# Optimization experiments

Measured on AMD Instinct MI355X. Metric: run time of the kernel, lower is better.

## Reference

```python
import jax, jax.numpy as jnp
import numpy as np

L = 4096          # total packed length
HID = 2560        # hidden_size
H = 8             # num_attention_heads
KV = 4            # num_key_value_heads
HD = 256          # head_dim
SW = 1024         # sliding_window
SCALING = 256.0 ** -0.5  # query_pre_attn_scalar ** -0.5
EPS = 1e-6
ROPE_BASE = 10000.0


def setup_inputs() -> dict:
    key = jax.random.key(0)
    ks = jax.random.split(key, 9)
    hidden_states = jax.random.normal(ks[0], (L, HID), jnp.float32)
    Wq = jax.random.normal(ks[1], (HID, H * HD), jnp.float32) * 0.02
    Wk = jax.random.normal(ks[2], (HID, KV * HD), jnp.float32) * 0.02
    Wv = jax.random.normal(ks[3], (HID, KV * HD), jnp.float32) * 0.02
    Wo = jax.random.normal(ks[4], (H * HD, HID), jnp.float32) * 0.02
    q_norm_w = jax.random.normal(ks[5], (HD,), jnp.float32) * 0.1
    k_norm_w = jax.random.normal(ks[6], (HD,), jnp.float32) * 0.1
    # 4 packed sequences of length 1024 each; positions restart per sequence
    cu_seqlens = jnp.array([0, 1024, 2048, 3072, 4096], jnp.int32)
    pos = jnp.tile(jnp.arange(1024, dtype=jnp.float32), 4)  # [L]
    inv_freq = 1.0 / (ROPE_BASE ** (jnp.arange(0, HD, 2, dtype=jnp.float32) / HD))
    freqs = pos[:, None] * inv_freq[None, :]                # [L, HD/2]
    emb = jnp.concatenate([freqs, freqs], axis=-1)          # [L, HD]
    cos, sin = jnp.cos(emb), jnp.sin(emb)
    return {"hidden_states": hidden_states, "cos": cos, "sin": sin,
            "Wq": Wq, "Wk": Wk, "Wv": Wv, "Wo": Wo,
            "q_norm_w": q_norm_w, "k_norm_w": k_norm_w,
            "cu_seqlens": cu_seqlens}


def _rotate_half(x):
    x1, x2 = x[..., : HD // 2], x[..., HD // 2:]
    return jnp.concatenate([-x2, x1], axis=-1)


def _rms_norm(x, w):
    # Gemma3RMSNorm: x * rsqrt(mean(x^2) + eps) * (1 + w)
    x32 = x.astype(jnp.float32)
    out = x32 * jax.lax.rsqrt(jnp.mean(x32 * x32, axis=-1, keepdims=True) + EPS)
    return (out * (1.0 + w.astype(jnp.float32))).astype(x.dtype)


def _packed_sliding_causal_mask(cu_seqlens, total_len):
    pos = jnp.arange(total_len)
    seq_ids = jnp.searchsorted(cu_seqlens[1:], pos, side='right')
    seq_mask = seq_ids[:, None] == seq_ids[None, :]
    dist = pos[None, :] - pos[:, None]                      # pos[j] - pos[i]
    causal = dist <= 0
    window = dist >= -(SW - 1)                              # left_window = SW - 1
    keep = seq_mask & causal & window
    return jnp.where(keep, 0.0, -jnp.inf).astype(jnp.float32)  # [L, L]


def reference(hidden_states, cos, sin, Wq, Wk, Wv, Wo, q_norm_w, k_norm_w, cu_seqlens):
    total_len = hidden_states.shape[0]
    # projections -> [n_heads, L, head_dim]
    q = (hidden_states @ Wq).reshape(total_len, H, HD).transpose(1, 0, 2)
    k = (hidden_states @ Wk).reshape(total_len, KV, HD).transpose(1, 0, 2)
    v = (hidden_states @ Wv).reshape(total_len, KV, HD).transpose(1, 0, 2)
    q = _rms_norm(q, q_norm_w)
    k = _rms_norm(k, k_norm_w)
    # RoPE (cos/sin broadcast over heads)
    q = q * cos + _rotate_half(q) * sin
    k = k * cos + _rotate_half(k) * sin
    # GQA repeat_kv: [KV, L, HD] -> [H, L, HD]
    n_rep = H // KV
    k = jnp.repeat(k, n_rep, axis=0)
    v = jnp.repeat(v, n_rep, axis=0)
    mask = _packed_sliding_causal_mask(cu_seqlens, total_len)
    scores = jnp.einsum('hqd,hkd->hqk', q, k) * SCALING + mask[None]
    attn = jax.nn.softmax(scores.astype(jnp.float32), axis=-1).astype(q.dtype)
    out = jnp.einsum('hqk,hkd->qhd', attn, v).reshape(total_len, H * HD)
    return out @ Wo  # [L, hidden]
```

## Files before the change

kernel.cpp:

```cpp
#include <hip/hip_runtime.h>
#include <hip/hip_bf16.h>

typedef unsigned short u16;
typedef float f32x4 __attribute__((ext_vector_type(4)));
typedef short bf16x8 __attribute__((ext_vector_type(8)));

__device__ __forceinline__ float bf2f(u16 u) {
    union { float f; unsigned int i; } c; c.i = ((unsigned int)u) << 16; return c.f;
}
__device__ __forceinline__ u16 f2bf(float f) {
    union { float f; unsigned int i; } c; c.f = f;
    unsigned int r = c.i + 0x7fffu + ((c.i >> 16) & 1u);
    return (u16)(r >> 16);
}
__device__ __forceinline__ void gload16(const void* g, void* l) {
    __builtin_amdgcn_global_load_lds(
        (const __attribute__((address_space(1))) void*)g,
        (__attribute__((address_space(3))) void*)l, 16, 0, 0);
}

__global__ __launch_bounds__(256) void convert_f32_bf16(
    const float* __restrict__ in, u16* __restrict__ out, int n8)
{
    int i = blockIdx.x * 256 + threadIdx.x;
    if (i >= n8) return;
    const float4 a = *(const float4*)&in[i * 8];
    const float4 b = *(const float4*)&in[i * 8 + 4];
    bf16x8 o;
    o[0] = (short)f2bf(a.x); o[1] = (short)f2bf(a.y);
    o[2] = (short)f2bf(a.z); o[3] = (short)f2bf(a.w);
    o[4] = (short)f2bf(b.x); o[5] = (short)f2bf(b.y);
    o[6] = (short)f2bf(b.z); o[7] = (short)f2bf(b.w);
    *(bf16x8*)&out[i * 8] = o;
}

__global__ __launch_bounds__(256) void transpose_f32_bf16(
    const float* __restrict__ in, u16* __restrict__ out, int R, int C)
{
    __shared__ u16 tile[32][34];
    const int tx = threadIdx.x & 31;
    const int ty = threadIdx.x >> 5;
    const size_t r0 = (size_t)blockIdx.y * 32;
    const size_t c0 = (size_t)blockIdx.x * 32;
#pragma unroll
    for (int i = 0; i < 4; ++i) {
        int r = ty + 8 * i;
        tile[r][tx] = f2bf(in[(r0 + r) * C + c0 + tx]);
    }
    __syncthreads();
#pragma unroll
    for (int i = 0; i < 4; ++i) {
        int r = ty + 8 * i;
        out[(c0 + r) * R + r0 + tx] = tile[tx][r];
    }
}

__global__ __launch_bounds__(256) void transpose_bf16(
    const u16* __restrict__ in, u16* __restrict__ out, int ldin, int ldout)
{
    __shared__ u16 tile[32][34];
    const int tx = threadIdx.x & 31;
    const int ty = threadIdx.x >> 5;
    const size_t r0 = (size_t)blockIdx.y * 32;
    const size_t c0 = (size_t)blockIdx.x * 32;
#pragma unroll
    for (int i = 0; i < 4; ++i) {
        int r = ty + 8 * i;
        tile[r][tx] = in[(r0 + r) * (size_t)ldin + c0 + tx];
    }
    __syncthreads();
#pragma unroll
    for (int i = 0; i < 4; ++i) {
        int r = ty + 8 * i;
        out[(c0 + r) * (size_t)ldout + r0 + tx] = tile[tx][r];
    }
}

template<typename TOUT>
__global__ __launch_bounds__(512, 2) void gemm_bt8p(
    const u16* __restrict__ A, const u16* __restrict__ Bt, TOUT* __restrict__ C,
    int M, int N, int K)
{
    __shared__ u16 As[2][2][128 * 64];
    __shared__ u16 Bs[2][2][128 * 64];
    const int tid  = threadIdx.x;
    const int lane = tid & 63;
    const int w    = tid >> 6;
    const int wm   = w >> 2;
    const int wn   = w & 3;
    const int g    = lane >> 4, c = lane & 15;

    const int nbx = gridDim.x;
    int lin = blockIdx.y * nbx + blockIdx.x;
    const int cpx = (nbx * gridDim.y) >> 3;
    lin = (lin & 7) * cpx + (lin >> 3);
    const size_t mbase = (size_t)(lin / nbx) * 256;
    const size_t nbase = (size_t)(lin % nbx) * 256;

    const int schunk = w * 2;
    const int srow0  = lane >> 3;
    const int sslot  = lane & 7;

    auto stageA = [&](int t, int half) {
        u16* dst = &As[t & 1][half][0];
        const u16* src = A + (mbase + half * 128) * (size_t)K + t * 64;
#pragma unroll
        for (int i = 0; i < 2; ++i) {
            const int ch = schunk + i;
            const int rw = ch * 8 + srow0;
            gload16(src + (size_t)rw * K + ((sslot ^ (rw & 7)) << 3), dst + ch * 512);
        }
    };
    auto stageB = [&](int t, int half) {
        u16* dst = &Bs[t & 1][half][0];
        const u16* src = Bt + (nbase + half * 128) * (size_t)K + t * 64;
#pragma unroll
        for (int i = 0; i < 2; ++i) {
            const int ch = schunk + i;
            const int rw = ch * 8 + srow0;
            gload16(src + (size_t)rw * K + ((sslot ^ (rw & 7)) << 3), dst + ch * 512);
        }
    };
    auto ldA = [&](int t, int m, int kk) -> bf16x8 {
        const int r = m * 16 + c;
        return *(const bf16x8*)&As[t & 1][wm][r * 64 + ((kk * 32 + g * 8) ^ ((r & 7) << 3))];
    };
    auto ldB = [&](int t, int n, int kk) -> bf16x8 {
        const int r = (wn & 1) * 64 + n * 16 + c;
        return *(const bf16x8*)&Bs[t & 1][wn >> 1][r * 64 + ((kk * 32 + g * 8) ^ ((r & 7) << 3))];
    };

    f32x4 acc[8][4];
#pragma unroll
    for (int m = 0; m < 8; ++m)
#pragma unroll
        for (int n = 0; n < 4; ++n) { acc[m][n][0]=0.f; acc[m][n][1]=0.f; acc[m][n][2]=0.f; acc[m][n][3]=0.f; }

    const int nT = K >> 6;

    stageA(0, 0); stageA(0, 1); stageB(0, 0); stageB(0, 1);
    asm volatile("s_waitcnt vmcnt(0)" ::: "memory");
    __builtin_amdgcn_sched_barrier(0);
    __builtin_amdgcn_s_barrier();

    for (int t = 0; t < nT; ++t) {
        bf16x8 bF[4][2], aF[2][2];
        const bool more = (t + 1 < nT);

#pragma unroll
        for (int n = 0; n < 4; ++n) { bF[n][0] = ldB(t, n, 0); bF[n][1] = ldB(t, n, 1); }
#pragma unroll
        for (int i = 0; i < 2; ++i) { aF[i][0] = ldA(t, i, 0); aF[i][1] = ldA(t, i, 1); }
        if (more) { stageA(t + 1, 0); stageA(t + 1, 1); }
        __builtin_amdgcn_s_barrier();
        __builtin_amdgcn_s_setprio(1);
#pragma unroll
        for (int kk = 0; kk < 2; ++kk)
#pragma unroll
            for (int i = 0; i < 2; ++i)
#pragma unroll
                for (int n = 0; n < 4; ++n)
                    acc[i][n] = __builtin_amdgcn_mfma_f32_16x16x32_bf16(
                        aF[i][kk], bF[n][kk], acc[i][n], 0, 0, 0);
        __builtin_amdgcn_s_setprio(0);
        __builtin_amdgcn_s_barrier();

#pragma unroll
        for (int q = 1; q < 4; ++q) {
#pragma unroll
            for (int i = 0; i < 2; ++i) { aF[i][0] = ldA(t, 2*q + i, 0); aF[i][1] = ldA(t, 2*q + i, 1); }
            if (q == 1 && more) { stageB(t + 1, 0); stageB(t + 1, 1); }
            __builtin_amdgcn_s_barrier();
            __builtin_amdgcn_s_setprio(1);
#pragma unroll
            for (int kk = 0; kk < 2; ++kk)
#pragma unroll
                for (int i = 0; i < 2; ++i)
#pragma unroll
                    for (int n = 0; n < 4; ++n)
                        acc[2*q + i][n] = __builtin_amdgcn_mfma_f32_16x16x32_bf16(
                            aF[i][kk], bF[n][kk], acc[2*q + i][n], 0, 0, 0);
            __builtin_amdgcn_s_setprio(0);
            __builtin_amdgcn_s_barrier();
        }

        asm volatile("s_waitcnt vmcnt(0)" ::: "memory");
        __builtin_amdgcn_sched_barrier(0);
        __builtin_amdgcn_s_barrier();
    }

#pragma unroll
    for (int m = 0; m < 8; ++m)
#pragma unroll
        for (int n = 0; n < 4; ++n)
#pragma unroll
            for (int i = 0; i < 4; ++i) {
                size_t r   = mbase + wm * 128 + m * 16 + g * 4 + i;
                size_t col = nbase + wn * 64 + n * 16 + c;
                if constexpr (sizeof(TOUT) == 4) C[r * (size_t)N + col] = acc[m][n][i];
                else                             C[r * (size_t)N + col] = f2bf(acc[m][n][i]);
            }
}

__global__ __launch_bounds__(256) void rmsnorm_rope(
    u16* __restrict__ buf, int ld, const float* __restrict__ wgt,
    const float* __restrict__ cosb, const float* __restrict__ sinb,
    int heads, float outscale)
{
    const int lane = threadIdx.x & 63;
    const int wv   = threadIdx.x >> 6;
    const int rid  = blockIdx.x * 4 + wv;
    const int t    = rid / heads;
    const int h    = rid - t * heads;
    u16* p = buf + (size_t)t * ld + h * 256 + lane * 4;

    ushort4 xu = *(const ushort4*)p;
    float x0 = bf2f(xu.x), x1 = bf2f(xu.y), x2 = bf2f(xu.z), x3 = bf2f(xu.w);
    float ss = x0*x0 + x1*x1 + x2*x2 + x3*x3;
#pragma unroll
    for (int msk = 1; msk < 64; msk <<= 1) ss += __shfl_xor(ss, msk);
    const float rstd = rsqrtf(ss * (1.0f / 256.0f) + 1e-6f);

    const int d0 = lane * 4;
    const float4 wv4 = *(const float4*)&wgt[d0];
    float xn0 = x0 * rstd * (1.0f + wv4.x);
    float xn1 = x1 * rstd * (1.0f + wv4.y);
    float xn2 = x2 * rstd * (1.0f + wv4.z);
    float xn3 = x3 * rstd * (1.0f + wv4.w);

    float pn0 = __shfl_xor(xn0, 32);
    float pn1 = __shfl_xor(xn1, 32);
    float pn2 = __shfl_xor(xn2, 32);
    float pn3 = __shfl_xor(xn3, 32);
    const float sgn = (lane < 32) ? -1.0f : 1.0f;

    const float4 cv = *(const float4*)&cosb[(size_t)t * 256 + d0];
    const float4 sv = *(const float4*)&sinb[(size_t)t * 256 + d0];
    float r0 = (xn0 * cv.x + sgn * pn0 * sv.x) * outscale;
    float r1 = (xn1 * cv.y + sgn * pn1 * sv.y) * outscale;
    float r2 = (xn2 * cv.z + sgn * pn2 * sv.z) * outscale;
    float r3 = (xn3 * cv.w + sgn * pn3 * sv.w) * outscale;

    ushort4 ou;
    ou.x = f2bf(r0); ou.y = f2bf(r1); ou.z = f2bf(r2); ou.w = f2bf(r3);
    *(ushort4*)p = ou;
}

__global__ __launch_bounds__(512) void attn_kernel(
    const u16* __restrict__ q, int ldq,
    const u16* __restrict__ k, int ldk,
    const u16* __restrict__ vT,
    u16* __restrict__ o)
{
    __shared__ u16 Ks[2][32 * 256];
    __shared__ u16 Vs[256 * 40];
    __shared__ u16 P[8][16][56];
    const int tid  = threadIdx.x;
    const int lane = tid & 63;
    const int w    = tid >> 6;
    const int g    = lane >> 4, c = lane & 15;
    const int qt   = 15 - blockIdx.x;
    const int s    = blockIdx.y;
    const int kvh  = blockIdx.z;
    const int h    = kvh * 2 + (w >> 2);
    const int seq0 = s << 10;
    const int qrow0 = qt * 64 + (w & 3) * 16;

    bf16x8 qf[8];
    {
        const u16* qp = q + (size_t)(seq0 + qrow0 + c) * ldq + h * 256 + g * 8;
#pragma unroll
        for (int ch = 0; ch < 8; ++ch) qf[ch] = *(const bf16x8*)(qp + ch * 32);
    }

    const int kchunk0  = w * 2;
    const int krow_in  = (lane >> 5);
    const int kcol_lin = (lane & 31) * 16;
    const u16* kbase = k + (size_t)seq0 * ldk + kvh * 256;
    const int vd  = tid & 255;
    const int vj0 = (tid >> 8) * 2;
    const int vsw = (vd >> 3) & 3;
    const u16* vbase = vT + ((size_t)kvh * 256 + vd) * 4096 + seq0 + vj0 * 8;

    f32x4 oacc[16];
#pragma unroll
    for (int dt = 0; dt < 16; ++dt) { oacc[dt][0]=0.f; oacc[dt][1]=0.f; oacc[dt][2]=0.f; oacc[dt][3]=0.f; }
    float m[4] = {-1e30f, -1e30f, -1e30f, -1e30f};
    float l[4] = {0.f, 0.f, 0.f, 0.f};

    const int nkv = 2 * (qt + 1);

    bf16x8 vreg[2];
#pragma unroll
    for (int i = 0; i < 2; ++i) {
        const int chunk = kchunk0 + i;
        const int row   = chunk * 2 + krow_in;
        const int bcol  = kcol_lin ^ ((row & 7) << 4);
        gload16(kbase + (size_t)row * ldk + (bcol >> 1), &Ks[0][chunk * 512]);
    }
#pragma unroll
    for (int j = 0; j < 2; ++j) vreg[j] = *(const bf16x8*)(vbase + j * 8);
    __syncthreads();
#pragma unroll
    for (int j = 0; j < 2; ++j)
        *(bf16x8*)&Vs[vd * 40 + (((vj0 + j) ^ vsw) * 8)] = vreg[j];
    __syncthreads();

    for (int kt = 0; kt < nkv; ++kt) {
        const int p   = kt & 1;
        const int kv0 = kt * 32;

        if (kt + 1 < nkv) {
#pragma unroll
            for (int i = 0; i < 2; ++i) {
                const int chunk = kchunk0 + i;
                const int row   = chunk * 2 + krow_in;
                const int bcol  = kcol_lin ^ ((row & 7) << 4);
                gload16(kbase + (size_t)(kv0 + 32 + row) * ldk + (bcol >> 1),
                        &Ks[p ^ 1][chunk * 512]);
            }
#pragma unroll
            for (int j = 0; j < 2; ++j) vreg[j] = *(const bf16x8*)(vbase + kv0 + 32 + j * 8);
        }

        f32x4 sacc[2];
#pragma unroll
        for (int nh = 0; nh < 2; ++nh) { sacc[nh][0]=0.f; sacc[nh][1]=0.f; sacc[nh][2]=0.f; sacc[nh][3]=0.f; }
        __builtin_amdgcn_s_setprio(1);
#pragma unroll
        for (int nh = 0; nh < 2; ++nh) {
            const int krow = nh * 16 + c;
#pragma unroll
            for (int ch = 0; ch < 8; ++ch) {
                const int sw = ((ch * 64 + g * 16) ^ ((c & 7) << 4)) >> 1;
                bf16x8 kf = *(const bf16x8*)&Ks[p][krow * 256 + sw];
                sacc[nh] = __builtin_amdgcn_mfma_f32_16x16x32_bf16(qf[ch], kf, sacc[nh], 0, 0, 0);
            }
        }
        __builtin_amdgcn_s_setprio(0);

        float corr[4];
#pragma unroll
        for (int i = 0; i < 4; ++i) {
            const int qi = qrow0 + g * 4 + i;
            if (kv0 + c      > qi) sacc[0][i] = -1e30f;
            if (kv0 + 16 + c > qi) sacc[1][i] = -1e30f;
            float v = fmaxf(sacc[0][i], sacc[1][i]);
            v = fmaxf(v, __shfl_xor(v, 1));
            v = fmaxf(v, __shfl_xor(v, 2));
            v = fmaxf(v, __shfl_xor(v, 4));
            v = fmaxf(v, __shfl_xor(v, 8));
            const float mn = fmaxf(m[i], v);
            corr[i] = __expf(m[i] - mn);
            m[i] = mn;
            const float p0 = __expf(sacc[0][i] - mn);
            const float p1 = __expf(sacc[1][i] - mn);
            float rs = p0 + p1;
            rs += __shfl_xor(rs, 1);
            rs += __shfl_xor(rs, 2);
            rs += __shfl_xor(rs, 4);
            rs += __shfl_xor(rs, 8);
            l[i] = l[i] * corr[i] + rs;
            P[w][g * 4 + i][c]      = f2bf(p0);
            P[w][g * 4 + i][c + 16] = f2bf(p1);
        }
        bf16x8 pf = *(const bf16x8*)&P[w][c][g * 8];

        __builtin_amdgcn_s_setprio(1);
#pragma unroll
        for (int dt = 0; dt < 16; ++dt) {
            const int d = dt * 16 + c;
            bf16x8 vf = *(const bf16x8*)&Vs[d * 40 + ((g ^ ((d >> 3) & 3)) * 8)];
#pragma unroll
            for (int i = 0; i < 4; ++i) oacc[dt][i] *= corr[i];
            oacc[dt] = __builtin_amdgcn_mfma_f32_16x16x32_bf16(pf, vf, oacc[dt], 0, 0, 0);
        }
        __builtin_amdgcn_s_setprio(0);

        __syncthreads();
        if (kt + 1 < nkv) {
#pragma unroll
            for (int j = 0; j < 2; ++j)
                *(bf16x8*)&Vs[vd * 40 + (((vj0 + j) ^ vsw) * 8)] = vreg[j];
        }
        __syncthreads();
    }

#pragma unroll
    for (int i = 0; i < 4; ++i) l[i] = 1.0f / l[i];
#pragma unroll
    for (int dt = 0; dt < 16; ++dt)
#pragma unroll
        for (int i = 0; i < 4; ++i)
            o[(size_t)(seq0 + qrow0 + g * 4 + i) * 2048 + h * 256 + dt * 16 + c] =
                f2bf(oacc[dt][i] * l[i]);
}

extern "C" void kernel_launch(void* const* d_in, const int* in_sizes, int n_in,
                              void* d_out, int out_size, void* d_ws, size_t ws_size,
                              hipStream_t stream)
{
    const float* hid  = (const float*)d_in[0];
    const float* cosb = (const float*)d_in[1];
    const float* sinb = (const float*)d_in[2];
    const float* Wq   = (const float*)d_in[3];
    const float* Wk   = (const float*)d_in[4];
    const float* Wv   = (const float*)d_in[5];
    const float* Wo   = (const float*)d_in[6];
    const float* qnw  = (const float*)d_in[7];
    const float* knw  = (const float*)d_in[8];

    char* ws = (char*)d_ws;
    const size_t R1 = 0;
    const size_t R2 = (size_t)4096 * 2560 * 2;
    const size_t R3 = R2 * 2;
    u16* hidb  = (u16*)(ws + R1);
    u16* WoT   = (u16*)(ws + R1);
    u16* vT    = (u16*)(ws + R1 + (size_t)2560 * 2048 * 2);
    u16* WqkvT = (u16*)(ws + R2);
    u16* ob    = (u16*)(ws + R2);
    u16* qkv   = (u16*)(ws + R3);
    (void)ws_size; (void)in_sizes; (void)n_in; (void)out_size;

    dim3 B(256);
    convert_f32_bf16<<<dim3(4096 * 2560 / 8 / 256), B, 0, stream>>>(hid, hidb, 4096 * 2560 / 8);
    transpose_f32_bf16<<<dim3(2048 / 32, 2560 / 32), B, 0, stream>>>(Wq, WqkvT, 2560, 2048);
    transpose_f32_bf16<<<dim3(1024 / 32, 2560 / 32), B, 0, stream>>>(Wk, WqkvT + (size_t)2048 * 2560, 2560, 1024);
    transpose_f32_bf16<<<dim3(1024 / 32, 2560 / 32), B, 0, stream>>>(Wv, WqkvT + (size_t)3072 * 2560, 2560, 1024);

    gemm_bt8p<u16><<<dim3(16, 16), dim3(512), 0, stream>>>(hidb, WqkvT, qkv, 4096, 4096, 2560);

    transpose_f32_bf16<<<dim3(2560 / 32, 2048 / 32), B, 0, stream>>>(Wo, WoT, 2048, 2560);

    rmsnorm_rope<<<dim3(8192), B, 0, stream>>>(qkv, 4096, qnw, cosb, sinb, 8, 0.0625f);
    rmsnorm_rope<<<dim3(4096), B, 0, stream>>>(qkv + 2048, 4096, knw, cosb, sinb, 4, 1.0f);

    transpose_bf16<<<dim3(1024 / 32, 4096 / 32), B, 0, stream>>>(qkv + 3072, vT, 4096, 4096);

    attn_kernel<<<dim3(16, 4, 4), dim3(512), 0, stream>>>(qkv, 4096, qkv + 2048, 4096, vT, ob);

    gemm_bt8p<float><<<dim3(10, 16), dim3(512), 0, stream>>>(ob, WoT, (float*)d_out, 4096, 2560, 2048);
}
```

Measured before the change: 295.5 us.

## Shrink attention blocks to 32 query rows and add lazy softmax rescaling

The attention kernel now uses 256-thread blocks covering 32 query rows, and the grid doubles to 32 query tiles. This gives more blocks, finer causal load balancing and less wasted masked work per block. The S=K·Q^T operand swap puts one query row per lane, so the row max and sum need only two cross-lane shuffles. Rescaling of the output accumulator is skipped unless the running max rises by more than 8, with the correction shared through LDS. The trade-off is that each block reloads K/V for fewer query rows, which adds global traffic, and the lazy rescale lets unnormalised values grow by up to e^8.

```diff
diff --git a/kernel.cpp b/kernel.cpp
--- a/kernel.cpp
+++ b/kernel.cpp
@@ -246,7 +246,7 @@
     *(ushort4*)p = ou;
 }
 
-__global__ __launch_bounds__(512) void attn_kernel(
+__global__ __launch_bounds__(256) void attn_kernel(
     const u16* __restrict__ q, int ldq,
     const u16* __restrict__ k, int ldk,
     const u16* __restrict__ vT,
@@ -254,17 +254,18 @@
 {
     __shared__ u16 Ks[2][32 * 256];
     __shared__ u16 Vs[256 * 40];
-    __shared__ u16 P[8][16][56];
+    __shared__ u16 P[4][16][56];
+    __shared__ float corrsF[4][16];
     const int tid  = threadIdx.x;
     const int lane = tid & 63;
     const int w    = tid >> 6;
     const int g    = lane >> 4, c = lane & 15;
-    const int qt   = 15 - blockIdx.x;
+    const int qt   = 31 - blockIdx.x;
     const int s    = blockIdx.y;
     const int kvh  = blockIdx.z;
-    const int h    = kvh * 2 + (w >> 2);
+    const int h    = kvh * 2 + (w >> 1);
     const int seq0 = s << 10;
-    const int qrow0 = qt * 64 + (w & 3) * 16;
+    const int qrow0 = qt * 32 + (w & 1) * 16;
 
     bf16x8 qf[8];
     {
@@ -273,37 +274,36 @@
         for (int ch = 0; ch < 8; ++ch) qf[ch] = *(const bf16x8*)(qp + ch * 32);
     }
 
-    const int kchunk0  = w * 2;
+    const int kchunk0  = w * 4;
     const int krow_in  = (lane >> 5);
     const int kcol_lin = (lane & 31) * 16;
     const u16* kbase = k + (size_t)seq0 * ldk + kvh * 256;
-    const int vd  = tid & 255;
-    const int vj0 = (tid >> 8) * 2;
+    const int vd  = tid;
     const int vsw = (vd >> 3) & 3;
-    const u16* vbase = vT + ((size_t)kvh * 256 + vd) * 4096 + seq0 + vj0 * 8;
+    const u16* vbase = vT + ((size_t)kvh * 256 + vd) * 4096 + seq0;
 
     f32x4 oacc[16];
 #pragma unroll
     for (int dt = 0; dt < 16; ++dt) { oacc[dt][0]=0.f; oacc[dt][1]=0.f; oacc[dt][2]=0.f; oacc[dt][3]=0.f; }
-    float m[4] = {-1e30f, -1e30f, -1e30f, -1e30f};
-    float l[4] = {0.f, 0.f, 0.f, 0.f};
-
-    const int nkv = 2 * (qt + 1);
-
-    bf16x8 vreg[2];
-#pragma unroll
-    for (int i = 0; i < 2; ++i) {
+    float mq = -1e30f;
+    float lq = 0.f;
+
+    const int nkv = qt + 1;
+
+    bf16x8 vreg[4];
+#pragma unroll
+    for (int i = 0; i < 4; ++i) {
         const int chunk = kchunk0 + i;
         const int row   = chunk * 2 + krow_in;
         const int bcol  = kcol_lin ^ ((row & 7) << 4);
         gload16(kbase + (size_t)row * ldk + (bcol >> 1), &Ks[0][chunk * 512]);
     }
 #pragma unroll
-    for (int j = 0; j < 2; ++j) vreg[j] = *(const bf16x8*)(vbase + j * 8);
+    for (int j = 0; j < 4; ++j) vreg[j] = *(const bf16x8*)(vbase + j * 8);
     __syncthreads();
 #pragma unroll
-    for (int j = 0; j < 2; ++j)
-        *(bf16x8*)&Vs[vd * 40 + (((vj0 + j) ^ vsw) * 8)] = vreg[j];
+    for (int j = 0; j < 4; ++j)
+        *(bf16x8*)&Vs[vd * 40 + ((j ^ vsw) * 8)] = vreg[j];
     __syncthreads();
 
     for (int kt = 0; kt < nkv; ++kt) {
@@ -312,7 +312,7 @@
 
         if (kt + 1 < nkv) {
 #pragma unroll
-            for (int i = 0; i < 2; ++i) {
+            for (int i = 0; i < 4; ++i) {
                 const int chunk = kchunk0 + i;
                 const int row   = chunk * 2 + krow_in;
                 const int bcol  = kcol_lin ^ ((row & 7) << 4);
@@ -320,7 +320,7 @@
                         &Ks[p ^ 1][chunk * 512]);
             }
 #pragma unroll
-            for (int j = 0; j < 2; ++j) vreg[j] = *(const bf16x8*)(vbase + kv0 + 32 + j * 8);
+            for (int j = 0; j < 4; ++j) vreg[j] = *(const bf16x8*)(vbase + kv0 + 32 + j * 8);
         }
 
         f32x4 sacc[2];
@@ -334,45 +334,68 @@
             for (int ch = 0; ch < 8; ++ch) {
                 const int sw = ((ch * 64 + g * 16) ^ ((c & 7) << 4)) >> 1;
                 bf16x8 kf = *(const bf16x8*)&Ks[p][krow * 256 + sw];
-                sacc[nh] = __builtin_amdgcn_mfma_f32_16x16x32_bf16(qf[ch], kf, sacc[nh], 0, 0, 0);
+                sacc[nh] = __builtin_amdgcn_mfma_f32_16x16x32_bf16(kf, qf[ch], sacc[nh], 0, 0, 0);
             }
         }
         __builtin_amdgcn_s_setprio(0);
 
-        float corr[4];
-#pragma unroll
-        for (int i = 0; i < 4; ++i) {
-            const int qi = qrow0 + g * 4 + i;
-            if (kv0 + c      > qi) sacc[0][i] = -1e30f;
-            if (kv0 + 16 + c > qi) sacc[1][i] = -1e30f;
-            float v = fmaxf(sacc[0][i], sacc[1][i]);
-            v = fmaxf(v, __shfl_xor(v, 1));
-            v = fmaxf(v, __shfl_xor(v, 2));
-            v = fmaxf(v, __shfl_xor(v, 4));
-            v = fmaxf(v, __shfl_xor(v, 8));
-            const float mn = fmaxf(m[i], v);
-            corr[i] = __expf(m[i] - mn);
-            m[i] = mn;
-            const float p0 = __expf(sacc[0][i] - mn);
-            const float p1 = __expf(sacc[1][i] - mn);
-            float rs = p0 + p1;
-            rs += __shfl_xor(rs, 1);
-            rs += __shfl_xor(rs, 2);
-            rs += __shfl_xor(rs, 4);
-            rs += __shfl_xor(rs, 8);
-            l[i] = l[i] * corr[i] + rs;
-            P[w][g * 4 + i][c]      = f2bf(p0);
-            P[w][g * 4 + i][c + 16] = f2bf(p1);
-        }
+        const int qloc = qrow0 + c;
+        float pmax = -1e30f;
+#pragma unroll
+        for (int nh = 0; nh < 2; ++nh)
+#pragma unroll
+            for (int i = 0; i < 4; ++i) {
+                if (kv0 + nh * 16 + g * 4 + i > qloc) sacc[nh][i] = -1e30f;
+                pmax = fmaxf(pmax, sacc[nh][i]);
+            }
+        pmax = fmaxf(pmax, __shfl_xor(pmax, 16));
+        pmax = fmaxf(pmax, __shfl_xor(pmax, 32));
+
+        const bool rescale = !__all(pmax - mq <= 8.0f);
+        float corr = 1.0f;
+        if (rescale) {
+            const float mn = fmaxf(mq, pmax);
+            corr = __expf(mq - mn);
+            mq = mn;
+            if (g == 0) corrsF[w][c] = corr;
+        }
+
+        float rowsum = 0.f;
+        unsigned int pw[4];
+#pragma unroll
+        for (int nh = 0; nh < 2; ++nh) {
+            float p0 = __expf(sacc[nh][0] - mq);
+            float p1 = __expf(sacc[nh][1] - mq);
+            float p2 = __expf(sacc[nh][2] - mq);
+            float p3 = __expf(sacc[nh][3] - mq);
+            rowsum += (p0 + p1) + (p2 + p3);
+            pw[nh * 2 + 0] = (unsigned int)f2bf(p0) | ((unsigned int)f2bf(p1) << 16);
+            pw[nh * 2 + 1] = (unsigned int)f2bf(p2) | ((unsigned int)f2bf(p3) << 16);
+        }
+#pragma unroll
+        for (int nh = 0; nh < 2; ++nh) {
+            *(unsigned int*)&P[w][c][nh * 16 + g * 4]     = pw[nh * 2 + 0];
+            *(unsigned int*)&P[w][c][nh * 16 + g * 4 + 2] = pw[nh * 2 + 1];
+        }
+        rowsum += __shfl_xor(rowsum, 16);
+        rowsum += __shfl_xor(rowsum, 32);
+        lq = lq * corr + rowsum;
+
         bf16x8 pf = *(const bf16x8*)&P[w][c][g * 8];
+
+        if (rescale) {
+            const f32x4 c4 = *(const f32x4*)&corrsF[w][g * 4];
+#pragma unroll
+            for (int dt = 0; dt < 16; ++dt)
+#pragma unroll
+                for (int i = 0; i < 4; ++i) oacc[dt][i] *= c4[i];
+        }
 
         __builtin_amdgcn_s_setprio(1);
 #pragma unroll
         for (int dt = 0; dt < 16; ++dt) {
             const int d = dt * 16 + c;
             bf16x8 vf = *(const bf16x8*)&Vs[d * 40 + ((g ^ ((d >> 3) & 3)) * 8)];
-#pragma unroll
-            for (int i = 0; i < 4; ++i) oacc[dt][i] *= corr[i];
             oacc[dt] = __builtin_amdgcn_mfma_f32_16x16x32_bf16(pf, vf, oacc[dt], 0, 0, 0);
         }
         __builtin_amdgcn_s_setprio(0);
@@ -380,20 +403,23 @@
         __syncthreads();
         if (kt + 1 < nkv) {
 #pragma unroll
-            for (int j = 0; j < 2; ++j)
-                *(bf16x8*)&Vs[vd * 40 + (((vj0 + j) ^ vsw) * 8)] = vreg[j];
+            for (int j = 0; j < 4; ++j)
+                *(bf16x8*)&Vs[vd * 40 + ((j ^ vsw) * 8)] = vreg[j];
         }
         __syncthreads();
     }
 
-#pragma unroll
-    for (int i = 0; i < 4; ++i) l[i] = 1.0f / l[i];
+    if (g == 0) corrsF[w][c] = lq;
+    const f32x4 l4 = *(const f32x4*)&corrsF[w][g * 4];
+    float linv[4];
+#pragma unroll
+    for (int i = 0; i < 4; ++i) linv[i] = 1.0f / l4[i];
 #pragma unroll
     for (int dt = 0; dt < 16; ++dt)
 #pragma unroll
         for (int i = 0; i < 4; ++i)
             o[(size_t)(seq0 + qrow0 + g * 4 + i) * 2048 + h * 256 + dt * 16 + c] =
-                f2bf(oacc[dt][i] * l[i]);
+                f2bf(oacc[dt][i] * linv[i]);
 }
 
 extern "C" void kernel_launch(void* const* d_in, const int* in_sizes, int n_in,
@@ -437,7 +463,7 @@
 
     transpose_bf16<<<dim3(1024 / 32, 4096 / 32), B, 0, stream>>>(qkv + 3072, vT, 4096, 4096);
 
-    attn_kernel<<<dim3(16, 4, 4), dim3(512), 0, stream>>>(qkv, 4096, qkv + 2048, 4096, vT, ob);
+    attn_kernel<<<dim3(32, 4, 4), dim3(256), 0, stream>>>(qkv, 4096, qkv + 2048, 4096, vT, ob);
 
     gemm_bt8p<float><<<dim3(10, 16), dim3(512), 0, stream>>>(ob, WoT, (float*)d_out, 4096, 2560, 2048);
 }
```

New measurement: 336.2 us. +13.8%, slower.
